# Kernel tuning notes

Hardware: AMD Instinct MI355X
Metric: run time of the kernel (lower is better)

Reference implementation:

```python
import jax, jax.numpy as jnp
import numpy as np

HEADS = 8
DIM_K = 64
DIM_G = 64
INPLANES = 512
PLANES = 128  # int(inplanes * ratio)


def setup_inputs() -> dict:
    key = jax.random.key(0)
    ks = jax.random.split(key, 12)
    B, C, H, W = 16, INPLANES, 64, 64
    s = lambda fan: 1.0 / np.sqrt(fan)
    return {
        "x": jax.random.normal(ks[0], (B, C, H, W), dtype=jnp.float32),
        # conv_mask: Conv2d(C, HEADS, 1)
        "conv_mask_w": jax.random.normal(ks[1], (HEADS, C), dtype=jnp.float32) * s(C),
        "conv_mask_b": jnp.zeros((HEADS,), dtype=jnp.float32),
        # LinearG: dim_g -> 1
        "g_w": jax.random.normal(ks[2], (1, DIM_G), dtype=jnp.float32) * s(DIM_G),
        "g_b": jnp.zeros((1,), dtype=jnp.float32),
        # LinearK/Q/V: C -> dim_k
        "k_w": jax.random.normal(ks[3], (DIM_K, C), dtype=jnp.float32) * s(C),
        "k_b": jnp.zeros((DIM_K,), dtype=jnp.float32),
        "q_w": jax.random.normal(ks[4], (DIM_K, C), dtype=jnp.float32) * s(C),
        "q_b": jnp.zeros((DIM_K,), dtype=jnp.float32),
        "v_w": jax.random.normal(ks[5], (DIM_K, C), dtype=jnp.float32) * s(C),
        "v_b": jnp.zeros((DIM_K,), dtype=jnp.float32),
        # channel_add_conv: Conv2d(H*dk, planes, 1) -> LN([planes,1,1]) -> ReLU -> Conv2d(planes, C, 1)
        "add_w1": jax.random.normal(ks[6], (PLANES, HEADS * DIM_K), dtype=jnp.float32) * s(HEADS * DIM_K),
        "add_b1": jnp.zeros((PLANES,), dtype=jnp.float32),
        "ln_g": jnp.ones((PLANES,), dtype=jnp.float32),
        "ln_b": jnp.zeros((PLANES,), dtype=jnp.float32),
        "add_w2": jax.random.normal(ks[7], (C, PLANES), dtype=jnp.float32) * s(PLANES),
        "add_b2": jnp.zeros((C,), dtype=jnp.float32),
    }


def _forward(x, conv_mask_w, conv_mask_b, g_w, g_b, k_w, k_b, q_w, q_b,
             v_w, v_b, add_w1, add_b1, ln_g, ln_b, add_w2, add_b2):
    B, C, H, W = x.shape
    Hn, dk = HEADS, DIM_K
    # --- attention pooling mask ---
    logits = jnp.einsum('bchw,nc->bnhw', x, conv_mask_w) + conv_mask_b[None, :, None, None]
    mask = jax.nn.softmax(logits.reshape(B, Hn, H * W), axis=2)        # [B,Hn,HW]
    # per-head pooled context: [B,Hn,C]
    context = jnp.einsum('bcn,bhn->bhc', x.reshape(B, C, H * W), mask)
    # --- geometric position embedding ---
    mask4 = mask.reshape(B, Hn, H, W)
    cols = jnp.arange(W, dtype=x.dtype)   # mesh[...,0] = column index j
    rows = jnp.arange(H, dtype=x.dtype)   # mesh[...,1] = row index i
    cx = jnp.einsum('bnhw,w->bn', mask4, cols) / H
    cy = jnp.einsum('bnhw,h->bn', mask4, rows) / W
    dx = cx[:, :, None] - cx[:, None, :]
    dy = cy[:, :, None] - cy[:, None, :]
    # [B,Hn,Hn,4]
    pos = jnp.stack([jax.nn.relu(dx), jax.nn.relu(-dx),
                     jax.nn.relu(dy), jax.nn.relu(-dy)], axis=3)
    nfreq = DIM_G // 8
    dim_mat = 1.0 / (1000.0 ** (jnp.arange(nfreq, dtype=x.dtype) / nfreq))
    mul = (100.0 * pos[..., None]) * dim_mat                            # [B,Hn,Hn,4,nfreq]
    mul = mul.reshape(B, Hn, Hn, 4 * nfreq)
    emb = jnp.concatenate([jnp.sin(mul), jnp.cos(mul)], axis=-1)        # [B,Hn,Hn,DIM_G]
    w_g = jax.nn.relu(jnp.einsum('bmnd,od->bmno', emb, g_w)[..., 0] + g_b[0])  # [B,Hn,Hn]
    # --- head-level attention ---
    w_k = context @ k_w.T + k_b                                         # [B,Hn,dk]
    w_q = context @ q_w.T + q_b
    w_v = context @ v_w.T + v_b
    scaled_dot = jnp.einsum('bmd,bnd->bmn', w_k, w_q) / np.sqrt(dk)
    w_mn = jax.nn.softmax(jnp.log(jnp.clip(w_g, 1e-6)) + scaled_dot, axis=1)
    out_ctx = jnp.einsum('bmn,bmd->bnd', w_mn, w_v).reshape(B, Hn * dk)  # [B,512]
    # --- channel_add fusion (1x1 conv -> LN -> ReLU -> 1x1 conv), spatial dims are 1 ---
    y = out_ctx @ add_w1.T + add_b1                                     # [B,PLANES]
    mu = jnp.mean(y, axis=-1, keepdims=True)
    var = jnp.mean((y - mu) ** 2, axis=-1, keepdims=True)
    y = (y - mu) / jnp.sqrt(var + 1e-5) * ln_g + ln_b
    y = jax.nn.relu(y)
    add_term = y @ add_w2.T + add_b2                                    # [B,C]
    return x + add_term[:, :, None, None]


def reference(x, conv_mask_w, conv_mask_b, g_w, g_b, k_w, k_b, q_w, q_b,
              v_w, v_b, add_w1, add_b1, ln_g, ln_b, add_w2, add_b2):
    return _forward(x, conv_mask_w, conv_mask_b, g_w, g_b, k_w, k_b, q_w, q_b,
                    v_w, v_b, add_w1, add_b1, ln_g, ln_b, add_w2, add_b2)
```

## Files before the change

kernel.cpp:

```cpp
#include <hip/hip_runtime.h>
#include <cmath>

#define BB 16
#define CC 512
#define HWH 4096
#define NH 8
#define DK 64
#define PL 128

typedef float fx4 __attribute__((ext_vector_type(4)));

__device__ __forceinline__ float wred_sum(float v){
#pragma unroll
  for (int m = 32; m >= 1; m >>= 1) v += __shfl_xor(v, m, 64);
  return v;
}

#define OFF_E     0
#define OFF_PSUM  524288
#define OFF_PCTX  532480
#define OFF_KQV   663552
#define OFF_ADDT  688128

__global__ __launch_bounds__(512) void k_logexp(const float* __restrict__ x,
                                                const float* __restrict__ cmw,
                                                float* __restrict__ e,
                                                float* __restrict__ psum) {
  __shared__ float lds[4 * NH * 64 * 4];
  int b = blockIdx.x >> 4, pt = blockIdx.x & 15;
  int t = threadIdx.x, cs = t >> 6, l = t & 63;
  int pbase = pt * 256;
  const float* xb = x + ((size_t)(b * CC + cs * 64)) * HWH + pbase + l * 4;
  const float* wb = cmw + cs * 64;
  float acc[NH][4];
#pragma unroll
  for (int n = 0; n < NH; n++)
#pragma unroll
    for (int k = 0; k < 4; k++) acc[n][k] = 0.f;
#pragma unroll 8
  for (int c = 0; c < 64; c++) {
    float4 xv = *reinterpret_cast<const float4*>(xb + (size_t)c * HWH);
#pragma unroll
    for (int n = 0; n < NH; n++) {
      float wv = wb[n * CC + c];
      acc[n][0] = fmaf(xv.x, wv, acc[n][0]);
      acc[n][1] = fmaf(xv.y, wv, acc[n][1]);
      acc[n][2] = fmaf(xv.z, wv, acc[n][2]);
      acc[n][3] = fmaf(xv.w, wv, acc[n][3]);
    }
  }
  auto stslot = [&](int s) {
#pragma unroll
    for (int n = 0; n < NH; n++)
#pragma unroll
      for (int k = 0; k < 4; k++)
        lds[((s * NH + n) * 64 + l) * 4 + k] = acc[n][k];
  };
  auto ldslot = [&](int s) {
#pragma unroll
    for (int n = 0; n < NH; n++)
#pragma unroll
      for (int k = 0; k < 4; k++)
        acc[n][k] += lds[((s * NH + n) * 64 + l) * 4 + k];
  };
  if (cs >= 4) stslot(cs - 4);
  __syncthreads();
  if (cs < 4) ldslot(cs);
  __syncthreads();
  if (cs == 2 || cs == 3) stslot(cs - 2);
  __syncthreads();
  if (cs < 2) ldslot(cs);
  __syncthreads();
  if (cs == 1) stslot(0);
  __syncthreads();
  if (cs == 0) {
    ldslot(0);
    int p0 = pbase + l * 4;
    float colf = (float)(p0 & 63);
    float rowf = (float)(p0 >> 6);
#pragma unroll
    for (int n = 0; n < NH; n++) {
      float4 ev;
      ev.x = expf(acc[n][0]); ev.y = expf(acc[n][1]);
      ev.z = expf(acc[n][2]); ev.w = expf(acc[n][3]);
      *reinterpret_cast<float4*>(e + (size_t)(b * NH + n) * HWH + p0) = ev;
      float s  = ev.x + ev.y + ev.z + ev.w;
      float sc = ev.x * colf + ev.y * (colf + 1.f) + ev.z * (colf + 2.f) + ev.w * (colf + 3.f);
      float sy = s * rowf;
      s = wred_sum(s); sc = wred_sum(sc); sy = wred_sum(sy);
      if (l == 0) {
        size_t base = (((size_t)(b * NH + n)) * 16 + pt) * 4;
        psum[base] = s; psum[base + 1] = sc; psum[base + 2] = sy;
      }
    }
  }
}

__global__ __launch_bounds__(512) void k_context(const float* __restrict__ x,
                                                 const float* __restrict__ e,
                                                 float* __restrict__ pctx) {
  int bid = blockIdx.x;
  int ng = bid & 1;
  int cg = (bid >> 1) & 15;
  int b = bid >> 5;
  int w = threadIdx.x >> 6;
  int l = threadIdx.x & 63;
  int cbase = cg * 32 + w * 4;
  const float* xb = x + ((size_t)(b * CC + cbase)) * HWH + ng * 2048 + l * 4;
  const float* eb = e + (size_t)b * NH * HWH + ng * 2048 + l * 4;
  float acc[4][NH];
#pragma unroll
  for (int ci = 0; ci < 4; ci++)
#pragma unroll
    for (int h = 0; h < NH; h++) acc[ci][h] = 0.f;
#pragma unroll 2
  for (int ch = 0; ch < 8; ch++) {
    int off = ch * 256;
    float4 ev[NH];
#pragma unroll
    for (int h = 0; h < NH; h++)
      ev[h] = *reinterpret_cast<const float4*>(eb + (size_t)h * HWH + off);
#pragma unroll
    for (int ci = 0; ci < 4; ci++) {
      float4 xv = *reinterpret_cast<const float4*>(xb + (size_t)ci * HWH + off);
#pragma unroll
      for (int h = 0; h < NH; h++) {
        float a = acc[ci][h];
        a = fmaf(xv.x, ev[h].x, a);
        a = fmaf(xv.y, ev[h].y, a);
        a = fmaf(xv.z, ev[h].z, a);
        a = fmaf(xv.w, ev[h].w, a);
        acc[ci][h] = a;
      }
    }
  }
#pragma unroll
  for (int ci = 0; ci < 4; ci++)
#pragma unroll
    for (int h = 0; h < NH; h++) acc[ci][h] = wred_sum(acc[ci][h]);
  if (l == 0) {
    float* op = pctx + ((size_t)(ng * BB + b) * NH) * CC + cbase;
#pragma unroll
    for (int h = 0; h < NH; h++)
#pragma unroll
      for (int ci = 0; ci < 4; ci++) op[h * CC + ci] = acc[ci][h];
  }
}

__global__ __launch_bounds__(512) void k_kqv(const float* __restrict__ pctx,
    const float* __restrict__ psum,
    const float* __restrict__ k_w, const float* __restrict__ q_w,
    const float* __restrict__ v_w,
    const float* __restrict__ k_b, const float* __restrict__ q_b,
    const float* __restrict__ v_b,
    float* __restrict__ kqvbuf) {
  int bid = blockIdx.x;
  int b = bid / 24;
  int r = bid - b * 24;
  int j = r >> 3;
  int h = r & 7;
  int t = threadIdx.x;
  __shared__ float ctx[8 * 68];
  __shared__ float psumS[64 * 9];
  __shared__ float invS_s;
  if (t < 16) {
    float S = psum[(((size_t)(b * NH + h)) * 16 + t) * 4];
#pragma unroll
    for (int m = 8; m >= 1; m >>= 1) S += __shfl_xor(S, m, 64);
    if (t == 0) invS_s = 1.f / S;
  }
  __syncthreads();
  float inv = invS_s;
  size_t base = ((size_t)b * NH + h) * CC + t;
  float cval = (pctx[base] + pctx[(size_t)BB * NH * CC + base]) * inv;
  ctx[(t >> 6) * 68 + (t & 63)] = cval;
  __syncthreads();
  const float* wm = (j == 0) ? k_w : (j == 1) ? q_w : v_w;
  const float* bm = (j == 0) ? k_b : (j == 1) ? q_b : v_b;
  int d = t >> 3, s = t & 7;
  const float* wr = wm + d * CC + s * 64;
  const float* cl = ctx + s * 68;
  float a = 0.f;
#pragma unroll
  for (int c = 0; c < 64; c += 4) {
    float4 w4 = *reinterpret_cast<const float4*>(wr + c);
    a = fmaf(w4.x, cl[c + 0], a);
    a = fmaf(w4.y, cl[c + 1], a);
    a = fmaf(w4.z, cl[c + 2], a);
    a = fmaf(w4.w, cl[c + 3], a);
  }
  psumS[d * 9 + s] = a;
  __syncthreads();
  if (t < 64) {
    float rsum = 0.f;
#pragma unroll
    for (int ss = 0; ss < 8; ss++) rsum += psumS[t * 9 + ss];
    kqvbuf[((size_t)(b * 3 + j) * NH + h) * DK + t] = rsum + bm[t];
  }
}

__global__ __launch_bounds__(512) void k_attn_mlp(const float* __restrict__ kqvbuf,
    const float* __restrict__ psum,
    const float* __restrict__ g_w, const float* __restrict__ g_b,
    const float* __restrict__ aw1, const float* __restrict__ ab1,
    const float* __restrict__ lng, const float* __restrict__ lnb,
    const float* __restrict__ aw2, const float* __restrict__ ab2,
    float* __restrict__ add_term) {
  int b = blockIdx.x;
  int t = threadIdx.x;
  int wv = t >> 6, l = t & 63;
  __shared__ float kq[3][NH * 68];
  __shared__ float smn[NH][NH];
  __shared__ float cxl[NH], cyl[NH];
  __shared__ float oc[CC];
  __shared__ float part[4][PL];
  __shared__ float yl[PL];
  __shared__ float sr[2][2];

  if (t < 128) {
    int h = t >> 4, pt = t & 15;
    size_t base = (((size_t)(b * NH + h)) * 16 + pt) * 4;
    float S = psum[base], SC = psum[base + 1], SY = psum[base + 2];
#pragma unroll
    for (int m = 8; m >= 1; m >>= 1) {
      S += __shfl_xor(S, m, 64); SC += __shfl_xor(SC, m, 64); SY += __shfl_xor(SY, m, 64);
    }
    if ((t & 15) == 0) {
      cxl[h] = SC / (S * 64.f);
      cyl[h] = SY / (S * 64.f);
    }
  }
  {
    int h = t >> 6, d = t & 63;
#pragma unroll
    for (int j = 0; j < 3; j++)
      kq[j][h * 68 + d] = kqvbuf[(size_t)(b * 3 + j) * 512 + t];
  }
  __syncthreads();

  if (t < 64) {
    int m = t >> 3, n = t & 7;
    float dx = cxl[m] - cxl[n];
    float dy = cyl[m] - cyl[n];
    float pos[4] = { fmaxf(dx, 0.f), fmaxf(-dx, 0.f), fmaxf(dy, 0.f), fmaxf(-dy, 0.f) };
    float a = g_b[0];
#pragma unroll
    for (int p = 0; p < 4; p++) {
#pragma unroll
      for (int f = 0; f < 8; f++) {
        float dm = expf(-0.8634694098727671f * (float)f);
        float ang = 100.f * pos[p] * dm;
        a = fmaf(sinf(ang), g_w[p * 8 + f], a);
        a = fmaf(cosf(ang), g_w[32 + p * 8 + f], a);
      }
    }
    float wgl = logf(fmaxf(fmaxf(a, 0.f), 1e-6f));
    float dot = 0.f;
#pragma unroll
    for (int dd = 0; dd < DK; dd++)
      dot = fmaf(kq[0][m * 68 + dd], kq[1][n * 68 + dd], dot);
    smn[m][n] = dot * 0.125f + wgl;
  }
  __syncthreads();
  if (t < 8) {
    float mx = -1e30f;
#pragma unroll
    for (int m = 0; m < NH; m++) mx = fmaxf(mx, smn[m][t]);
    float ssum = 0.f; float ex[NH];
#pragma unroll
    for (int m = 0; m < NH; m++) { ex[m] = expf(smn[m][t] - mx); ssum += ex[m]; }
#pragma unroll
    for (int m = 0; m < NH; m++) smn[m][t] = ex[m] / ssum;
  }
  __syncthreads();
  {
    int n = t >> 6, d = t & 63;
    float a = 0.f;
#pragma unroll
    for (int m = 0; m < NH; m++) a = fmaf(smn[m][n], kq[2][m * 68 + d], a);
    oc[t] = a;
  }
  __syncthreads();
  {
    int d = t & 127, pq = t >> 7;
    const float* wr = aw1 + d * CC + pq * 128;
    const float* ol = oc + pq * 128;
    float a = 0.f;
#pragma unroll 8
    for (int c = 0; c < 128; c += 4) {
      float4 w4 = *reinterpret_cast<const float4*>(wr + c);
      a = fmaf(w4.x, ol[c + 0], a);
      a = fmaf(w4.y, ol[c + 1], a);
      a = fmaf(w4.z, ol[c + 2], a);
      a = fmaf(w4.w, ol[c + 3], a);
    }
    part[pq][d] = a;
  }
  __syncthreads();
  float y = 0.f;
  if (t < PL) y = part[0][t] + part[1][t] + part[2][t] + part[3][t] + ab1[t];
  {
    float s  = (t < PL) ? y : 0.f;
    float sq = s * y;
    s = wred_sum(s); sq = wred_sum(sq);
    if (t < PL && l == 0) { sr[0][wv] = s; sr[1][wv] = sq; }
  }
  __syncthreads();
  {
    float mu = (sr[0][0] + sr[0][1]) * (1.f / 128.f);
    float var = (sr[1][0] + sr[1][1]) * (1.f / 128.f) - mu * mu;
    float rstd = rsqrtf(var + 1e-5f);
    if (t < PL) yl[t] = fmaxf((y - mu) * rstd * lng[t] + lnb[t], 0.f);
  }
  __syncthreads();
  {
    const float* wr = aw2 + t * PL;
    float a = ab2[t];
#pragma unroll 8
    for (int pp = 0; pp < PL; pp += 4) {
      float4 w4 = *reinterpret_cast<const float4*>(wr + pp);
      a = fmaf(w4.x, yl[pp + 0], a);
      a = fmaf(w4.y, yl[pp + 1], a);
      a = fmaf(w4.z, yl[pp + 2], a);
      a = fmaf(w4.w, yl[pp + 3], a);
    }
    add_term[b * CC + t] = a;
  }
}

__global__ __launch_bounds__(256) void k_add(const float* __restrict__ x,
                                             const float* __restrict__ add_term,
                                             float* __restrict__ out) {
  const fx4* x4 = reinterpret_cast<const fx4*>(x);
  fx4* o4 = reinterpret_cast<fx4*>(out);
  const size_t n4 = (size_t)BB * CC * HWH / 4;
  for (size_t i = (size_t)blockIdx.x * 256 + threadIdx.x; i < n4;
       i += (size_t)gridDim.x * 256) {
    fx4 v = x4[i];
    float a = add_term[i >> 10];
    v += a;
    __builtin_nontemporal_store(v, &o4[i]);
  }
}

extern "C" void kernel_launch(void* const* d_in, const int* in_sizes, int n_in,
                              void* d_out, int out_size, void* d_ws, size_t ws_size,
                              hipStream_t stream) {
  const float* x   = (const float*)d_in[0];
  const float* cmw = (const float*)d_in[1];
  const float* g_w = (const float*)d_in[3];
  const float* g_b = (const float*)d_in[4];
  const float* k_w = (const float*)d_in[5];
  const float* k_b = (const float*)d_in[6];
  const float* q_w = (const float*)d_in[7];
  const float* q_b = (const float*)d_in[8];
  const float* v_w = (const float*)d_in[9];
  const float* v_b = (const float*)d_in[10];
  const float* aw1 = (const float*)d_in[11];
  const float* ab1 = (const float*)d_in[12];
  const float* lng = (const float*)d_in[13];
  const float* lnb = (const float*)d_in[14];
  const float* aw2 = (const float*)d_in[15];
  const float* ab2 = (const float*)d_in[16];
  float* out = (float*)d_out;
  float* ws = (float*)d_ws;

  float* e    = ws + OFF_E;
  float* psum = ws + OFF_PSUM;
  float* pctx = ws + OFF_PCTX;
  float* kqvb = ws + OFF_KQV;
  float* addt = ws + OFF_ADDT;

  hipLaunchKernelGGL(k_logexp,   dim3(256),  dim3(512), 0, stream, x, cmw, e, psum);
  hipLaunchKernelGGL(k_context,  dim3(512),  dim3(512), 0, stream, x, e, pctx);
  hipLaunchKernelGGL(k_kqv,      dim3(384),  dim3(512), 0, stream, pctx, psum,
                     k_w, q_w, v_w, k_b, q_b, v_b, kqvb);
  hipLaunchKernelGGL(k_attn_mlp, dim3(16),   dim3(512), 0, stream, kqvb, psum,
                     g_w, g_b, aw1, ab1, lng, lnb, aw2, ab2, addt);
  hipLaunchKernelGGL(k_add,      dim3(2048), dim3(256), 0, stream, x, addt, out);
}
```

Before: 147.5 us.

## Fuse mask-logit/exp and context pooling into one front kernel via LDS

Merges the logit+exp kernel and the context-pooling kernel into one. Each block keeps its exp tile in shared memory and immediately computes partial context over its own channel slice of x, which it already streamed. This drops the intermediate e write/read and the second full pass over x (128 MB). The cost is a per-channel wavefront reduction of 8 values with serialized shuffles, and 16 spatial partials per context that k_kqv now has to sum instead of 2.

After: 178.8 us. 1.21x slower.

```diff
diff --git a/kernel.cpp b/kernel.cpp
--- a/kernel.cpp
+++ b/kernel.cpp
@@ -16,17 +16,17 @@
   return v;
 }
 
-#define OFF_E     0
-#define OFF_PSUM  524288
-#define OFF_PCTX  532480
-#define OFF_KQV   663552
-#define OFF_ADDT  688128
-
-__global__ __launch_bounds__(512) void k_logexp(const float* __restrict__ x,
-                                                const float* __restrict__ cmw,
-                                                float* __restrict__ e,
-                                                float* __restrict__ psum) {
+#define OFF_PCTX  0
+#define OFF_PSUM  1048576
+#define OFF_KQV   1056768
+#define OFF_ADDT  1081344
+
+__global__ __launch_bounds__(512) void k_front(const float* __restrict__ x,
+                                               const float* __restrict__ cmw,
+                                               float* __restrict__ pctx,
+                                               float* __restrict__ psum) {
   __shared__ float lds[4 * NH * 64 * 4];
+  __shared__ float e_lds[NH][256];
   int b = blockIdx.x >> 4, pt = blockIdx.x & 15;
   int t = threadIdx.x, cs = t >> 6, l = t & 63;
   int pbase = pt * 256;
@@ -83,7 +83,7 @@
       float4 ev;
       ev.x = expf(acc[n][0]); ev.y = expf(acc[n][1]);
       ev.z = expf(acc[n][2]); ev.w = expf(acc[n][3]);
-      *reinterpret_cast<float4*>(e + (size_t)(b * NH + n) * HWH + p0) = ev;
+      *reinterpret_cast<float4*>(&e_lds[n][l * 4]) = ev;
       float s  = ev.x + ev.y + ev.z + ev.w;
       float sc = ev.x * colf + ev.y * (colf + 1.f) + ev.z * (colf + 2.f) + ev.w * (colf + 3.f);
       float sy = s * rowf;
@@ -94,56 +94,33 @@
       }
     }
   }
-}
-
-__global__ __launch_bounds__(512) void k_context(const float* __restrict__ x,
-                                                 const float* __restrict__ e,
-                                                 float* __restrict__ pctx) {
-  int bid = blockIdx.x;
-  int ng = bid & 1;
-  int cg = (bid >> 1) & 15;
-  int b = bid >> 5;
-  int w = threadIdx.x >> 6;
-  int l = threadIdx.x & 63;
-  int cbase = cg * 32 + w * 4;
-  const float* xb = x + ((size_t)(b * CC + cbase)) * HWH + ng * 2048 + l * 4;
-  const float* eb = e + (size_t)b * NH * HWH + ng * 2048 + l * 4;
-  float acc[4][NH];
-#pragma unroll
-  for (int ci = 0; ci < 4; ci++)
-#pragma unroll
-    for (int h = 0; h < NH; h++) acc[ci][h] = 0.f;
+  __syncthreads();
+
+  {
+    float4 ev[NH];
+#pragma unroll
+    for (int h = 0; h < NH; h++)
+      ev[h] = *reinterpret_cast<const float4*>(&e_lds[h][l * 4]);
+    float* op = pctx + (((size_t)(pt * BB + b)) * NH) * CC + cs * 64;
 #pragma unroll 2
-  for (int ch = 0; ch < 8; ch++) {
-    int off = ch * 256;
-    float4 ev[NH];
-#pragma unroll
-    for (int h = 0; h < NH; h++)
-      ev[h] = *reinterpret_cast<const float4*>(eb + (size_t)h * HWH + off);
-#pragma unroll
-    for (int ci = 0; ci < 4; ci++) {
-      float4 xv = *reinterpret_cast<const float4*>(xb + (size_t)ci * HWH + off);
+    for (int ci = 0; ci < 64; ci++) {
+      float4 xv = *reinterpret_cast<const float4*>(xb + (size_t)ci * HWH);
+      float a[NH];
 #pragma unroll
       for (int h = 0; h < NH; h++) {
-        float a = acc[ci][h];
-        a = fmaf(xv.x, ev[h].x, a);
-        a = fmaf(xv.y, ev[h].y, a);
-        a = fmaf(xv.z, ev[h].z, a);
-        a = fmaf(xv.w, ev[h].w, a);
-        acc[ci][h] = a;
+        float s = xv.x * ev[h].x;
+        s = fmaf(xv.y, ev[h].y, s);
+        s = fmaf(xv.z, ev[h].z, s);
+        s = fmaf(xv.w, ev[h].w, s);
+        a[h] = s;
       }
-    }
-  }
-#pragma unroll
-  for (int ci = 0; ci < 4; ci++)
-#pragma unroll
-    for (int h = 0; h < NH; h++) acc[ci][h] = wred_sum(acc[ci][h]);
-  if (l == 0) {
-    float* op = pctx + ((size_t)(ng * BB + b) * NH) * CC + cbase;
-#pragma unroll
-    for (int h = 0; h < NH; h++)
-#pragma unroll
-      for (int ci = 0; ci < 4; ci++) op[h * CC + ci] = acc[ci][h];
+#pragma unroll
+      for (int h = 0; h < NH; h++) a[h] = wred_sum(a[h]);
+      if (l == 0) {
+#pragma unroll
+        for (int h = 0; h < NH; h++) op[h * CC + ci] = a[h];
+      }
+    }
   }
 }
 
@@ -172,8 +149,15 @@
   __syncthreads();
   float inv = invS_s;
   size_t base = ((size_t)b * NH + h) * CC + t;
-  float cval = (pctx[base] + pctx[(size_t)BB * NH * CC + base]) * inv;
-  ctx[(t >> 6) * 68 + (t & 63)] = cval;
+  float c0 = 0.f, c1 = 0.f, c2 = 0.f, c3 = 0.f;
+#pragma unroll
+  for (int pt = 0; pt < 16; pt += 4) {
+    c0 += pctx[(size_t)(pt + 0) * BB * NH * CC + base];
+    c1 += pctx[(size_t)(pt + 1) * BB * NH * CC + base];
+    c2 += pctx[(size_t)(pt + 2) * BB * NH * CC + base];
+    c3 += pctx[(size_t)(pt + 3) * BB * NH * CC + base];
+  }
+  ctx[(t >> 6) * 68 + (t & 63)] = (c0 + c1 + c2 + c3) * inv;
   __syncthreads();
   const float* wm = (j == 0) ? k_w : (j == 1) ? q_w : v_w;
   const float* bm = (j == 0) ? k_b : (j == 1) ? q_b : v_b;
@@ -365,14 +349,12 @@
   float* out = (float*)d_out;
   float* ws = (float*)d_ws;
 
-  float* e    = ws + OFF_E;
+  float* pctx = ws + OFF_PCTX;
   float* psum = ws + OFF_PSUM;
-  float* pctx = ws + OFF_PCTX;
   float* kqvb = ws + OFF_KQV;
   float* addt = ws + OFF_ADDT;
 
-  hipLaunchKernelGGL(k_logexp,   dim3(256),  dim3(512), 0, stream, x, cmw, e, psum);
-  hipLaunchKernelGGL(k_context,  dim3(512),  dim3(512), 0, stream, x, e, pctx);
+  hipLaunchKernelGGL(k_front,    dim3(256),  dim3(512), 0, stream, x, cmw, pctx, psum);
   hipLaunchKernelGGL(k_kqv,      dim3(384),  dim3(512), 0, stream, pctx, psum,
                      k_w, q_w, v_w, k_b, q_b, v_b, kqvb);
   hipLaunchKernelGGL(k_attn_mlp, dim3(16),   dim3(512), 0, stream, kqvb, psum,
```

## Use wave-reduction matvecs in kqv and split attn_mlp final projection across blocks

Applied to the files above, without the earlier changes.

The k_kqv and aw1 matvecs are reorganized so each wavefront reads contiguous weight rows and reduces with cross-lane shuffles, which drops the shared-memory partial sums and a barrier. k_attn_mlp now launches 8 blocks per batch, each producing 64 of the 512 output channels with coalesced float2 weight reads, so the final projection spreads over many more CUs. The cost is that each of the 8 blocks recomputes the attention and first MLP layer for its batch.

Measured after the change: 144.6 us. Within noise of the previous version (-1.9%).

```diff
diff --git a/kernel.cpp b/kernel.cpp
--- a/kernel.cpp
+++ b/kernel.cpp
@@ -159,9 +159,8 @@
   int r = bid - b * 24;
   int j = r >> 3;
   int h = r & 7;
-  int t = threadIdx.x;
-  __shared__ float ctx[8 * 68];
-  __shared__ float psumS[64 * 9];
+  int t = threadIdx.x, wv = t >> 6, l = t & 63;
+  __shared__ float ctx[512];
   __shared__ float invS_s;
   if (t < 16) {
     float S = psum[(((size_t)(b * NH + h)) * 16 + t) * 4];
@@ -172,30 +171,23 @@
   __syncthreads();
   float inv = invS_s;
   size_t base = ((size_t)b * NH + h) * CC + t;
-  float cval = (pctx[base] + pctx[(size_t)BB * NH * CC + base]) * inv;
-  ctx[(t >> 6) * 68 + (t & 63)] = cval;
-  __syncthreads();
+  ctx[t] = (pctx[base] + pctx[(size_t)BB * NH * CC + base]) * inv;
+  __syncthreads();
+  float4 c0 = *reinterpret_cast<const float4*>(&ctx[l * 8]);
+  float4 c1 = *reinterpret_cast<const float4*>(&ctx[l * 8 + 4]);
   const float* wm = (j == 0) ? k_w : (j == 1) ? q_w : v_w;
   const float* bm = (j == 0) ? k_b : (j == 1) ? q_b : v_b;
-  int d = t >> 3, s = t & 7;
-  const float* wr = wm + d * CC + s * 64;
-  const float* cl = ctx + s * 68;
-  float a = 0.f;
-#pragma unroll
-  for (int c = 0; c < 64; c += 4) {
-    float4 w4 = *reinterpret_cast<const float4*>(wr + c);
-    a = fmaf(w4.x, cl[c + 0], a);
-    a = fmaf(w4.y, cl[c + 1], a);
-    a = fmaf(w4.z, cl[c + 2], a);
-    a = fmaf(w4.w, cl[c + 3], a);
-  }
-  psumS[d * 9 + s] = a;
-  __syncthreads();
-  if (t < 64) {
-    float rsum = 0.f;
-#pragma unroll
-    for (int ss = 0; ss < 8; ss++) rsum += psumS[t * 9 + ss];
-    kqvbuf[((size_t)(b * 3 + j) * NH + h) * DK + t] = rsum + bm[t];
+#pragma unroll
+  for (int i = 0; i < 8; i++) {
+    int d = wv * 8 + i;
+    const float* wr = wm + d * CC + l * 8;
+    float4 w0 = *reinterpret_cast<const float4*>(wr);
+    float4 w1 = *reinterpret_cast<const float4*>(wr + 4);
+    float a = w0.x * c0.x + w0.y * c0.y + w0.z * c0.z + w0.w * c0.w
+            + w1.x * c1.x + w1.y * c1.y + w1.z * c1.z + w1.w * c1.w;
+    a = wred_sum(a);
+    if (l == 0)
+      kqvbuf[((size_t)(b * 3 + j) * NH + h) * DK + d] = a + bm[d];
   }
 }
 
@@ -206,14 +198,15 @@
     const float* __restrict__ lng, const float* __restrict__ lnb,
     const float* __restrict__ aw2, const float* __restrict__ ab2,
     float* __restrict__ add_term) {
-  int b = blockIdx.x;
+  int b = blockIdx.x >> 3;
+  int slice = blockIdx.x & 7;
   int t = threadIdx.x;
   int wv = t >> 6, l = t & 63;
   __shared__ float kq[3][NH * 68];
   __shared__ float smn[NH][NH];
   __shared__ float cxl[NH], cyl[NH];
   __shared__ float oc[CC];
-  __shared__ float part[4][PL];
+  __shared__ float ypre[PL];
   __shared__ float yl[PL];
   __shared__ float sr[2][2];
 
@@ -282,23 +275,23 @@
   }
   __syncthreads();
   {
-    int d = t & 127, pq = t >> 7;
-    const float* wr = aw1 + d * CC + pq * 128;
-    const float* ol = oc + pq * 128;
-    float a = 0.f;
-#pragma unroll 8
-    for (int c = 0; c < 128; c += 4) {
-      float4 w4 = *reinterpret_cast<const float4*>(wr + c);
-      a = fmaf(w4.x, ol[c + 0], a);
-      a = fmaf(w4.y, ol[c + 1], a);
-      a = fmaf(w4.z, ol[c + 2], a);
-      a = fmaf(w4.w, ol[c + 3], a);
-    }
-    part[pq][d] = a;
+    float4 o0 = *reinterpret_cast<const float4*>(&oc[l * 8]);
+    float4 o1 = *reinterpret_cast<const float4*>(&oc[l * 8 + 4]);
+#pragma unroll
+    for (int i = 0; i < 16; i++) {
+      int d = wv * 16 + i;
+      const float* wr = aw1 + d * CC + l * 8;
+      float4 w0 = *reinterpret_cast<const float4*>(wr);
+      float4 w1 = *reinterpret_cast<const float4*>(wr + 4);
+      float a = w0.x * o0.x + w0.y * o0.y + w0.z * o0.z + w0.w * o0.w
+              + w1.x * o1.x + w1.y * o1.y + w1.z * o1.z + w1.w * o1.w;
+      a = wred_sum(a);
+      if (l == 0) ypre[d] = a + ab1[d];
+    }
   }
   __syncthreads();
   float y = 0.f;
-  if (t < PL) y = part[0][t] + part[1][t] + part[2][t] + part[3][t] + ab1[t];
+  if (t < PL) y = ypre[t];
   {
     float s  = (t < PL) ? y : 0.f;
     float sq = s * y;
@@ -314,17 +307,15 @@
   }
   __syncthreads();
   {
-    const float* wr = aw2 + t * PL;
-    float a = ab2[t];
-#pragma unroll 8
-    for (int pp = 0; pp < PL; pp += 4) {
-      float4 w4 = *reinterpret_cast<const float4*>(wr + pp);
-      a = fmaf(w4.x, yl[pp + 0], a);
-      a = fmaf(w4.y, yl[pp + 1], a);
-      a = fmaf(w4.z, yl[pp + 2], a);
-      a = fmaf(w4.w, yl[pp + 3], a);
-    }
-    add_term[b * CC + t] = a;
+    float2 yv = *reinterpret_cast<const float2*>(&yl[l * 2]);
+#pragma unroll
+    for (int i = 0; i < 8; i++) {
+      int c = slice * 64 + wv * 8 + i;
+      float2 w2 = *reinterpret_cast<const float2*>(aw2 + c * PL + l * 2);
+      float a = w2.x * yv.x + w2.y * yv.y;
+      a = wred_sum(a);
+      if (l == 0) add_term[b * CC + c] = a + ab2[c];
+    }
   }
 }
 
@@ -375,7 +366,7 @@
   hipLaunchKernelGGL(k_context,  dim3(512),  dim3(512), 0, stream, x, e, pctx);
   hipLaunchKernelGGL(k_kqv,      dim3(384),  dim3(512), 0, stream, pctx, psum,
                      k_w, q_w, v_w, k_b, q_b, v_b, kqvb);
-  hipLaunchKernelGGL(k_attn_mlp, dim3(16),   dim3(512), 0, stream, kqvb, psum,
+  hipLaunchKernelGGL(k_attn_mlp, dim3(128),  dim3(512), 0, stream, kqvb, psum,
                      g_w, g_b, aw1, ab1, lng, lnb, aw2, ab2, addt);
   hipLaunchKernelGGL(k_add,      dim3(2048), dim3(256), 0, stream, x, addt, out);
 }
```
